# Performance work log

Measured on AMD Instinct MI355X. Metric: run time of the kernel, lower is better.

The kernel has to match this reference:

```python
import jax, jax.numpy as jnp
import numpy as np

# BERT-base dims; 768 and max_sent_num=64 come from the module/config.
N, S, V, D, L, H, F = 8, 512, 30522, 768, 12, 12, 3072
DH = D // H
MAX_SENT = 64
LN_EPS = 1e-12
SCALE = float(np.sqrt(DH))


def _ln(x, g, b):
    m = jnp.mean(x, axis=-1, keepdims=True)
    v = jnp.mean(jnp.square(x - m), axis=-1, keepdims=True)
    return (x - m) * jax.lax.rsqrt(v + LN_EPS) * g + b


def setup_inputs() -> dict:
    key = jax.random.key(0)
    ks = jax.random.split(key, 10)
    # random token ids in a range avoiding the special ids 102/103
    ids = jax.random.randint(ks[0], (N, S), 999, 30000, dtype=jnp.int32)
    # variable per-doc sentence region -> ragged number of [MASK](103) separators (8..64)
    cutoff = jax.random.randint(ks[1], (N, 1), 64, S + 1)
    pos = jnp.arange(S)[None, :]
    sent_pos = ((pos % 8) == 7) & (pos < cutoff)
    ids = jnp.where(sent_pos, 103, ids)
    ids = ids.at[:, 0].set(102)  # exactly one [SEP]=102 per doc (required by the slice-assign)
    amask = jnp.ones((N, S), dtype=jnp.int32)
    g = lambda k, shape: 0.02 * jax.random.normal(k, shape, dtype=jnp.float32)
    inp = dict(input_ids_bert=ids, attention_mask_bert=amask)
    inp["tok_emb"] = g(ks[2], (V, D))
    inp["pos_emb"] = g(ks[3], (S, D))
    inp["emb_ln_g"] = jnp.ones((D,), jnp.float32)
    inp["emb_ln_b"] = jnp.zeros((D,), jnp.float32)
    inp["Wqkv"] = g(ks[4], (L, D, 3 * D))
    inp["bqkv"] = jnp.zeros((L, 3 * D), jnp.float32)
    inp["Wo"] = g(ks[5], (L, D, D))
    inp["bo"] = jnp.zeros((L, D), jnp.float32)
    inp["ln1_g"] = jnp.ones((L, D), jnp.float32)
    inp["ln1_b"] = jnp.zeros((L, D), jnp.float32)
    inp["W1"] = g(ks[6], (L, D, F))
    inp["b1"] = jnp.zeros((L, F), jnp.float32)
    inp["W2"] = g(ks[7], (L, F, D))
    inp["b2"] = jnp.zeros((L, D), jnp.float32)
    inp["ln2_g"] = jnp.ones((L, D), jnp.float32)
    inp["ln2_b"] = jnp.zeros((L, D), jnp.float32)
    return inp


def _bert(ids, amask, tok_emb, pos_emb, emb_ln_g, emb_ln_b,
          Wqkv, bqkv, Wo, bo, ln1_g, ln1_b, W1, b1, W2, b2, ln2_g, ln2_b):
    x = tok_emb[ids] + pos_emb[None, :, :]            # [N,S,D]
    x = _ln(x, emb_ln_g, emb_ln_b)
    bias = (1.0 - amask[:, None, None, :].astype(x.dtype)) * -1e9  # [N,1,1,S]

    def layer(x, p):
        wqkv, bq, wo, bo_, g1, b1n, w1, b1f, w2, b2f, g2, b2n = p
        qkv = x @ wqkv + bq
        q, k, v = jnp.split(qkv, 3, axis=-1)
        q = q.reshape(N, S, H, DH)
        k = k.reshape(N, S, H, DH)
        v = v.reshape(N, S, H, DH)
        att = jnp.einsum('bqhd,bkhd->bhqk', q, k) / SCALE + bias
        att = jax.nn.softmax(att, axis=-1)
        o = jnp.einsum('bhqk,bkhd->bqhd', att, v).reshape(N, S, D)
        x2 = _ln(x + o @ wo + bo_, g1, b1n)
        h = jax.nn.gelu(x2 @ w1 + b1f, approximate=False)
        return _ln(x2 + h @ w2 + b2f, g2, b2n), None

    x, _ = jax.lax.scan(layer, x, (Wqkv, bqkv, Wo, bo, ln1_g, ln1_b, W1, b1, W2, b2, ln2_g, ln2_b))
    return x


def _gather_scatter(ids, h):
    # Vectorized form of the per-doc python loop:
    #   out[doc, :n_sent] = concat([cls_emb(102), sent_embs(103)])[:-1]
    mask_sent = ids == 103
    mask_cls = ids == 102
    n_cls = mask_cls.sum(axis=1, keepdims=True)              # == 1 per doc
    total_sent = mask_sent.sum(axis=1, keepdims=True)        # ragged count
    rank_sent = jnp.cumsum(mask_sent, axis=1) - 1
    rank_cls = jnp.cumsum(mask_cls, axis=1) - 1
    dest = jnp.where(mask_cls, rank_cls,
                     jnp.where(mask_sent, n_cls + rank_sent, MAX_SENT))
    valid = (mask_cls | mask_sent) & (dest < total_sent) & (dest < MAX_SENT)
    dest_safe = jnp.where(valid, dest, MAX_SENT)             # dump invalid into scratch row
    vals = jnp.where(valid[..., None], h, 0.0)
    out = jnp.zeros((ids.shape[0], MAX_SENT + 1, D), dtype=h.dtype)
    out = out.at[jnp.arange(ids.shape[0])[:, None], dest_safe].set(vals)
    return out[:, :MAX_SENT]


def reference(input_ids_bert, attention_mask_bert, tok_emb, pos_emb, emb_ln_g, emb_ln_b,
              Wqkv, bqkv, Wo, bo, ln1_g, ln1_b, W1, b1, W2, b2, ln2_g, ln2_b):
    h = _bert(input_ids_bert, attention_mask_bert, tok_emb, pos_emb, emb_ln_g, emb_ln_b,
              Wqkv, bqkv, Wo, bo, ln1_g, ln1_b, W1, b1, W2, b2, ln2_g, ln2_b)
    return _gather_scatter(input_ids_bert, h)
```

## Files before the change

### kernel.cpp

```cpp
#include <hip/hip_runtime.h>
#include <hip/hip_bf16.h>

#define DEV static __device__ __forceinline__

using short8 = __attribute__((ext_vector_type(8))) short;
using f32x4 = __attribute__((ext_vector_type(4))) float;

DEV short f2bf(float f) {
  union { float f; unsigned u; } x; x.f = f;
  unsigned r = x.u + 0x7fffu + ((x.u >> 16) & 1u);
  return (short)(r >> 16);
}

DEV float bf2f(short s) {
  union { unsigned u; float f; } x; x.u = ((unsigned)(unsigned short)s) << 16;
  return x.f;
}

DEV void gload16(const void* g, void* lds) {
  __builtin_amdgcn_global_load_lds(
      (const __attribute__((address_space(1))) void*)g,
      (__attribute__((address_space(3))) void*)lds, 16, 0, 0);
}

__global__ __launch_bounds__(256) void transpose_all_k(
    const float* __restrict__ Wqkv, const float* __restrict__ Wo,
    const float* __restrict__ W1, const float* __restrict__ W2,
    short* __restrict__ wqkvT, short* __restrict__ woT,
    short* __restrict__ w1T, short* __restrict__ w2T)
{
  __shared__ short t[64][72];
  const int b = blockIdx.x, tid = threadIdx.x;
  const float* in; short* out; int K, N, tt, nt;
  if (b < 432)       { in = Wqkv; out = wqkvT; K = 768;  N = 2304; tt = b;        nt = 36; }
  else if (b < 576)  { in = Wo;   out = woT;   K = 768;  N = 768;  tt = b - 432;  nt = 12; }
  else if (b < 1152) { in = W1;   out = w1T;   K = 768;  N = 3072; tt = b - 576;  nt = 48; }
  else               { in = W2;   out = w2T;   K = 3072; N = 768;  tt = b - 1152; nt = 12; }
  const int n0 = (tt % nt) * 64, k0 = (tt / nt) * 64;
  #pragma unroll
  for (int p = 0; p < 4; ++p) {
    int r = p * 16 + (tid >> 4), c4 = tid & 15;
    float4 v = *reinterpret_cast<const float4*>(in + (size_t)(k0 + r) * N + n0 + c4 * 4);
    t[r][c4 * 4 + 0] = f2bf(v.x);
    t[r][c4 * 4 + 1] = f2bf(v.y);
    t[r][c4 * 4 + 2] = f2bf(v.z);
    t[r][c4 * 4 + 3] = f2bf(v.w);
  }
  __syncthreads();
  #pragma unroll
  for (int q = 0; q < 2; ++q) {
    int n = tid >> 2, kc = (tid & 3) + q * 4;
    short8 o;
    #pragma unroll
    for (int j = 0; j < 8; ++j) o[j] = t[kc * 8 + j][n];
    *reinterpret_cast<short8*>(out + (size_t)(n0 + n) * K + k0 + kc * 8) = o;
  }
}

template <int BM, int EPI>
__global__ __launch_bounds__(256) void gemm_bt(
    const short* __restrict__ A, const short* __restrict__ Bt,
    const float* __restrict__ bias, const float* __restrict__ resid,
    void* __restrict__ Cout, int M, int Nn, int K)
{
  constexpr int AW = BM / 64;
  constexpr int MI = BM / 32;
  __shared__ short As[2 * BM * 32];
  __shared__ short Bs[2 * 128 * 32];
  const int tid = threadIdx.x, lane = tid & 63, w = tid >> 6;
  const int wr = w >> 1, wc = w & 1;
  const int l15 = lane & 15, l4 = lane >> 4;
  const int m0 = blockIdx.y * BM, n0 = blockIdx.x * 128;
  const int crow = lane >> 2, ccol = (lane & 3) * 8;

  f32x4 acc[MI][4] = {};

  for (int k0 = 0; k0 < K; k0 += 64) {
    #pragma unroll
    for (int ks = 0; ks < 2; ++ks) {
      #pragma unroll
      for (int s = 0; s < AW; ++s) {
        int c = w * AW + s;
        gload16(A + (size_t)(m0 + c * 16 + crow) * K + k0 + ks * 32 + ccol,
                &As[ks * BM * 32 + c * 512]);
      }
      #pragma unroll
      for (int s = 0; s < 2; ++s) {
        int c = w * 2 + s;
        gload16(Bt + (size_t)(n0 + c * 16 + crow) * K + k0 + ks * 32 + ccol,
                &Bs[ks * 128 * 32 + c * 512]);
      }
    }
    __syncthreads();

    #pragma unroll
    for (int ks = 0; ks < 2; ++ks) {
      short8 af[MI], bfr[4];
      #pragma unroll
      for (int i = 0; i < MI; ++i)
        af[i] = *reinterpret_cast<const short8*>(
            &As[ks * BM * 32 + (wr * (BM / 2) + i * 16 + l15) * 32 + l4 * 8]);
      #pragma unroll
      for (int j = 0; j < 4; ++j)
        bfr[j] = *reinterpret_cast<const short8*>(
            &Bs[ks * 128 * 32 + (wc * 64 + j * 16 + l15) * 32 + l4 * 8]);
      #pragma unroll
      for (int i = 0; i < MI; ++i)
        #pragma unroll
        for (int j = 0; j < 4; ++j)
          acc[i][j] = __builtin_amdgcn_mfma_f32_16x16x32_bf16(af[i], bfr[j], acc[i][j], 0, 0, 0);
    }
    __syncthreads();
  }

  #pragma unroll
  for (int i = 0; i < MI; ++i) {
    #pragma unroll
    for (int j = 0; j < 4; ++j) {
      #pragma unroll
      for (int r = 0; r < 4; ++r) {
        int row = m0 + wr * (BM / 2) + i * 16 + l4 * 4 + r;
        int col = n0 + wc * 64 + j * 16 + l15;
        float v = acc[i][j][r] + bias[col];
        if constexpr (EPI == 1) v = 0.5f * v * (1.0f + erff(v * 0.70710678118654752f));
        ((short*)Cout)[(size_t)row * Nn + col] = f2bf(v);
      }
    }
  }
}

__global__ __launch_bounds__(256) void gemm_sk(
    const short* __restrict__ A, const short* __restrict__ Bt,
    short* __restrict__ p0, short* __restrict__ p1,
    short* __restrict__ p2, short* __restrict__ p3,
    int M, int Nn, int Kstride, int Klen)
{
  __shared__ short As[2 * 128 * 32];
  __shared__ short Bs[2 * 128 * 32];
  const int tid = threadIdx.x, lane = tid & 63, w = tid >> 6;
  const int wr = w >> 1, wc = w & 1;
  const int l15 = lane & 15, l4 = lane >> 4;
  const int m0 = blockIdx.y * 128, n0 = blockIdx.x * 128;
  const int koff = blockIdx.z * Klen;
  const int crow = lane >> 2, ccol = (lane & 3) * 8;

  f32x4 acc[4][4] = {};

  for (int k0 = 0; k0 < Klen; k0 += 64) {
    #pragma unroll
    for (int ks = 0; ks < 2; ++ks) {
      #pragma unroll
      for (int s = 0; s < 2; ++s) {
        int c = w * 2 + s;
        gload16(A + (size_t)(m0 + c * 16 + crow) * Kstride + koff + k0 + ks * 32 + ccol,
                &As[ks * 4096 + c * 512]);
      }
      #pragma unroll
      for (int s = 0; s < 2; ++s) {
        int c = w * 2 + s;
        gload16(Bt + (size_t)(n0 + c * 16 + crow) * Kstride + koff + k0 + ks * 32 + ccol,
                &Bs[ks * 4096 + c * 512]);
      }
    }
    __syncthreads();

    #pragma unroll
    for (int ks = 0; ks < 2; ++ks) {
      short8 af[4], bfr[4];
      #pragma unroll
      for (int i = 0; i < 4; ++i)
        af[i] = *reinterpret_cast<const short8*>(
            &As[ks * 4096 + (wr * 64 + i * 16 + l15) * 32 + l4 * 8]);
      #pragma unroll
      for (int j = 0; j < 4; ++j)
        bfr[j] = *reinterpret_cast<const short8*>(
            &Bs[ks * 4096 + (wc * 64 + j * 16 + l15) * 32 + l4 * 8]);
      #pragma unroll
      for (int i = 0; i < 4; ++i)
        #pragma unroll
        for (int j = 0; j < 4; ++j)
          acc[i][j] = __builtin_amdgcn_mfma_f32_16x16x32_bf16(af[i], bfr[j], acc[i][j], 0, 0, 0);
    }
    __syncthreads();
  }

  short* P = (blockIdx.z == 0) ? p0 : (blockIdx.z == 1) ? p1 : (blockIdx.z == 2) ? p2 : p3;
  #pragma unroll
  for (int i = 0; i < 4; ++i)
    #pragma unroll
    for (int j = 0; j < 4; ++j)
      #pragma unroll
      for (int r = 0; r < 4; ++r) {
        int row = m0 + wr * 64 + i * 16 + l4 * 4 + r;
        int col = n0 + wc * 64 + j * 16 + l15;
        P[(size_t)row * Nn + col] = f2bf(acc[i][j][r]);
      }
}

__global__ __launch_bounds__(256) void attn_k(
    const short* __restrict__ qkv, const int* __restrict__ amask,
    short* __restrict__ out)
{
  __shared__ short Kl[64][72];
  __shared__ short Vt[64][68];
  __shared__ short Pl[4][16][72];
  const int b = blockIdx.z, h = blockIdx.y, qt = blockIdx.x;
  const int tid = threadIdx.x, lane = tid & 63, w = tid >> 6;
  const int l15 = lane & 15, l4 = lane >> 4;
  const int tok0 = b * 512;
  const int q0 = qt * 64 + w * 16;

  short8 qf[2];
  #pragma unroll
  for (int kk = 0; kk < 2; ++kk)
    qf[kk] = *reinterpret_cast<const short8*>(
        qkv + (size_t)(tok0 + q0 + l15) * 2304 + h * 64 + kk * 32 + l4 * 8);

  f32x4 oacc[4] = {};
  float mrow[4], lrow[4];
  #pragma unroll
  for (int r = 0; r < 4; ++r) { mrow[r] = -1e30f; lrow[r] = 0.f; }

  for (int kt0 = 0; kt0 < 512; kt0 += 64) {
    #pragma unroll
    for (int i = 0; i < 2; ++i) {
      int c = tid + i * 256;
      int r = c >> 3, dc = c & 7;
      short8 v = *reinterpret_cast<const short8*>(
          qkv + (size_t)(tok0 + kt0 + r) * 2304 + 768 + h * 64 + dc * 8);
      *reinterpret_cast<short8*>(&Kl[r][dc * 8]) = v;
    }
    #pragma unroll
    for (int i = 0; i < 2; ++i) {
      int c = tid + i * 256;
      int r = c >> 3, dc = c & 7;
      short8 v = *reinterpret_cast<const short8*>(
          qkv + (size_t)(tok0 + kt0 + r) * 2304 + 1536 + h * 64 + dc * 8);
      #pragma unroll
      for (int j = 0; j < 8; ++j) Vt[dc * 8 + j][r] = v[j];
    }
    __syncthreads();

    f32x4 sacc[4] = {};
    #pragma unroll
    for (int t = 0; t < 4; ++t) {
      #pragma unroll
      for (int kk = 0; kk < 2; ++kk) {
        short8 kf = *reinterpret_cast<const short8*>(&Kl[t * 16 + l15][kk * 32 + l4 * 8]);
        sacc[t] = __builtin_amdgcn_mfma_f32_16x16x32_bf16(qf[kk], kf, sacc[t], 0, 0, 0);
      }
    }
    float p[4][4];
    #pragma unroll
    for (int t = 0; t < 4; ++t) {
      int ktok = kt0 + t * 16 + l15;
      float biasv = amask[b * 512 + ktok] ? 0.f : -1e9f;
      #pragma unroll
      for (int r = 0; r < 4; ++r) p[t][r] = sacc[t][r] * 0.125f + biasv;
    }
    #pragma unroll
    for (int r = 0; r < 4; ++r) {
      float mx = fmaxf(fmaxf(p[0][r], p[1][r]), fmaxf(p[2][r], p[3][r]));
      #pragma unroll
      for (int s = 1; s <= 8; s <<= 1) mx = fmaxf(mx, __shfl_xor(mx, s, 64));
      float mnew = fmaxf(mrow[r], mx);
      float alpha = __expf(mrow[r] - mnew);
      mrow[r] = mnew;
      float sum = 0.f;
      #pragma unroll
      for (int t = 0; t < 4; ++t) { p[t][r] = __expf(p[t][r] - mnew); sum += p[t][r]; }
      #pragma unroll
      for (int s = 1; s <= 8; s <<= 1) sum += __shfl_xor(sum, s, 64);
      lrow[r] = lrow[r] * alpha + sum;
      #pragma unroll
      for (int t = 0; t < 4; ++t) oacc[t][r] *= alpha;
    }
    #pragma unroll
    for (int t = 0; t < 4; ++t)
      #pragma unroll
      for (int r = 0; r < 4; ++r)
        Pl[w][l4 * 4 + r][t * 16 + l15] = f2bf(p[t][r]);
    #pragma unroll
    for (int kk = 0; kk < 2; ++kk) {
      short8 pf = *reinterpret_cast<const short8*>(&Pl[w][l15][kk * 32 + l4 * 8]);
      #pragma unroll
      for (int t = 0; t < 4; ++t) {
        const unsigned* vp = reinterpret_cast<const unsigned*>(&Vt[t * 16 + l15][0]);
        union { short8 s; unsigned u[4]; } vu;
        #pragma unroll
        for (int w2 = 0; w2 < 4; ++w2) vu.u[w2] = vp[kk * 16 + l4 * 4 + w2];
        oacc[t] = __builtin_amdgcn_mfma_f32_16x16x32_bf16(pf, vu.s, oacc[t], 0, 0, 0);
      }
    }
    __syncthreads();
  }

  #pragma unroll
  for (int t = 0; t < 4; ++t)
    #pragma unroll
    for (int r = 0; r < 4; ++r) {
      int tok = tok0 + q0 + l4 * 4 + r;
      int dh = t * 16 + l15;
      out[(size_t)tok * 768 + h * 64 + dh] = f2bf(oacc[t][r] / lrow[r]);
    }
}

__global__ __launch_bounds__(256) void ln2_k(
    const short* __restrict__ p0, const short* __restrict__ p1,
    const short* __restrict__ p2, const short* __restrict__ p3,
    const float* __restrict__ bias, const float* __restrict__ resid,
    const float* __restrict__ g, const float* __restrict__ be,
    float* __restrict__ xf, short* __restrict__ xb)
{
  const int t = blockIdx.x, tid = threadIdx.x;
  const size_t base = (size_t)t * 768;
  float v[3], s = 0.f, ss = 0.f;
  #pragma unroll
  for (int i = 0; i < 3; ++i) {
    int c = tid + i * 256;
    v[i] = (bf2f(p0[base + c]) + bf2f(p1[base + c]))
         + (bf2f(p2[base + c]) + bf2f(p3[base + c]))
         + bias[c] + resid[base + c];
    s += v[i]; ss += v[i] * v[i];
  }
  __shared__ float red[4][2];
  #pragma unroll
  for (int m = 1; m <= 32; m <<= 1) { s += __shfl_xor(s, m, 64); ss += __shfl_xor(ss, m, 64); }
  int w = tid >> 6;
  if ((tid & 63) == 0) { red[w][0] = s; red[w][1] = ss; }
  __syncthreads();
  s = red[0][0] + red[1][0] + red[2][0] + red[3][0];
  ss = red[0][1] + red[1][1] + red[2][1] + red[3][1];
  float mean = s * (1.f / 768.f);
  float var = ss * (1.f / 768.f) - mean * mean;
  float rs = rsqrtf(var + 1e-12f);
  #pragma unroll
  for (int i = 0; i < 3; ++i) {
    int c = tid + i * 256;
    float o = (v[i] - mean) * rs * g[c] + be[c];
    xf[base + c] = o;
    xb[base + c] = f2bf(o);
  }
}

__global__ __launch_bounds__(256) void embed_ln_k(
    const int* __restrict__ ids, const float* __restrict__ tok_emb,
    const float* __restrict__ pos_emb, const float* __restrict__ g,
    const float* __restrict__ be, float* __restrict__ xf, short* __restrict__ xb)
{
  const int t = blockIdx.x, tid = threadIdx.x;
  const int id = ids[t], sp = t & 511;
  float v[3], s = 0.f, ss = 0.f;
  #pragma unroll
  for (int i = 0; i < 3; ++i) {
    int c = tid + i * 256;
    v[i] = tok_emb[(size_t)id * 768 + c] + pos_emb[(size_t)sp * 768 + c];
    s += v[i]; ss += v[i] * v[i];
  }
  __shared__ float red[4][2];
  #pragma unroll
  for (int m = 1; m <= 32; m <<= 1) { s += __shfl_xor(s, m, 64); ss += __shfl_xor(ss, m, 64); }
  int w = tid >> 6;
  if ((tid & 63) == 0) { red[w][0] = s; red[w][1] = ss; }
  __syncthreads();
  s = red[0][0] + red[1][0] + red[2][0] + red[3][0];
  ss = red[0][1] + red[1][1] + red[2][1] + red[3][1];
  float mean = s * (1.f / 768.f);
  float var = ss * (1.f / 768.f) - mean * mean;
  float rs = rsqrtf(var + 1e-12f);
  #pragma unroll
  for (int i = 0; i < 3; ++i) {
    int c = tid + i * 256;
    float o = (v[i] - mean) * rs * g[c] + be[c];
    xf[(size_t)t * 768 + c] = o;
    xb[(size_t)t * 768 + c] = f2bf(o);
  }
}

__global__ __launch_bounds__(512) void gather_k(
    const int* __restrict__ ids, const float* __restrict__ x, float* __restrict__ out)
{
  const int doc = blockIdx.x, tid = threadIdx.x;
  const int lane = tid & 63, w = tid >> 6;
  __shared__ int src[64];
  __shared__ int wave_sent[8];
  __shared__ int cls_pos;
  if (tid < 64) src[tid] = -1;
  if (tid == 0) cls_pos = 0x7fffffff;
  __syncthreads();

  const int id = ids[doc * 512 + tid];
  const bool is_sent = (id == 103);
  const unsigned long long m = __ballot(is_sent);
  if (lane == 0) wave_sent[w] = __popcll(m);
  if (id == 102) atomicMin(&cls_pos, tid);
  __syncthreads();

  int total = 0, prefix = 0;
  #pragma unroll
  for (int i = 0; i < 8; ++i) {
    int c = wave_sent[i];
    if (i < w) prefix += c;
    total += c;
  }
  if (is_sent) {
    unsigned long long lt = lane ? (~0ULL >> (64 - lane)) : 0ULL;
    int d = 1 + prefix + __popcll(m & lt);
    if (d < total && d < 64) src[d] = tid;
  }
  if (tid == 0 && total > 0 && cls_pos != 0x7fffffff) src[0] = cls_pos;
  __syncthreads();

  for (int i = tid; i < 64 * 192; i += 512) {
    int row = i / 192, c4 = i - row * 192;
    int sp = src[row];
    float4 v = make_float4(0.f, 0.f, 0.f, 0.f);
    if (sp >= 0)
      v = reinterpret_cast<const float4*>(x + (size_t)(doc * 512 + sp) * 768)[c4];
    reinterpret_cast<float4*>(out + (size_t)doc * 64 * 768)[i] = v;
  }
}

extern "C" void kernel_launch(void* const* d_in, const int* in_sizes, int n_in,
                              void* d_out, int out_size, void* d_ws, size_t ws_size,
                              hipStream_t stream)
{
  const int* ids = (const int*)d_in[0];
  const int* am = (const int*)d_in[1];
  const float* tok_emb = (const float*)d_in[2];
  const float* pos_emb = (const float*)d_in[3];
  const float* eg = (const float*)d_in[4];
  const float* eb = (const float*)d_in[5];
  const float* Wqkv = (const float*)d_in[6];
  const float* bqkv = (const float*)d_in[7];
  const float* Wo = (const float*)d_in[8];
  const float* bo = (const float*)d_in[9];
  const float* g1 = (const float*)d_in[10];
  const float* b1n = (const float*)d_in[11];
  const float* W1 = (const float*)d_in[12];
  const float* b1f = (const float*)d_in[13];
  const float* W2 = (const float*)d_in[14];
  const float* b2f = (const float*)d_in[15];
  const float* g2 = (const float*)d_in[16];
  const float* b2n = (const float*)d_in[17];

  char* ws = (char*)d_ws;
  float* x_f   = (float*)(ws);
  short* x_b   = (short*)(ws + 12582912);
  float* x2_f  = (float*)(ws + 18874368);
  short* x2_b  = (short*)(ws + 31457280);
  short* pp0   = (short*)(ws + 37748736);
  short* pp1   = (short*)(ws + 37748736 + 6291456);
  short* qkv   = (short*)(ws + 50331648);
  short* pp2   = (short*)(ws + 50331648);
  short* pp3   = (short*)(ws + 50331648 + 6291456);
  short* attn  = (short*)(ws + 69206016);
  short* hb    = (short*)(ws + 75497472);
  short* wqkvT = (short*)(ws + 100663296);
  short* woT   = (short*)(ws + 104202240);
  short* w1T   = (short*)(ws + 105381888);
  short* w2T   = (short*)(ws + 110100480);

  embed_ln_k<<<4096, 256, 0, stream>>>(ids, tok_emb, pos_emb, eg, eb, x_f, x_b);

  for (int l = 0; l < 12; ++l) {
    transpose_all_k<<<1728, 256, 0, stream>>>(
        Wqkv + (size_t)l * 768 * 2304, Wo + (size_t)l * 768 * 768,
        W1 + (size_t)l * 768 * 3072, W2 + (size_t)l * 3072 * 768,
        wqkvT, woT, w1T, w2T);

    gemm_bt<128, 0><<<dim3(18, 32), 256, 0, stream>>>(
        x_b, wqkvT, bqkv + (size_t)l * 2304, nullptr, qkv, 4096, 2304, 768);
    attn_k<<<dim3(8, 12, 8), 256, 0, stream>>>(qkv, am, attn);

    gemm_sk<<<dim3(6, 32, 4), 256, 0, stream>>>(
        attn, woT, pp0, pp1, pp2, pp3, 4096, 768, 768, 192);
    ln2_k<<<4096, 256, 0, stream>>>(
        pp0, pp1, pp2, pp3, bo + (size_t)l * 768, x_f,
        g1 + (size_t)l * 768, b1n + (size_t)l * 768, x2_f, x2_b);

    gemm_bt<128, 1><<<dim3(24, 32), 256, 0, stream>>>(
        x2_b, w1T, b1f + (size_t)l * 3072, nullptr, hb, 4096, 3072, 768);

    gemm_sk<<<dim3(6, 32, 4), 256, 0, stream>>>(
        hb, w2T, pp0, pp1, pp2, pp3, 4096, 768, 3072, 768);
    ln2_k<<<4096, 256, 0, stream>>>(
        pp0, pp1, pp2, pp3, b2f + (size_t)l * 768, x2_f,
        g2 + (size_t)l * 768, b2n + (size_t)l * 768, x_f, x_b);
  }

  gather_k<<<8, 512, 0, stream>>>(ids, x_f, (float*)d_out);
}
```

Measured before the change: 2.208 ms.

## Batch weight transposes, swizzle workgroups across XCDs, use fast erf in GELU

When the workspace is large enough, all 12 layers' weights are transposed to bf16 in one launch up front, replacing a transpose launch per layer. GEMM and attention kernels remap their block indices with an XCD-aware swizzle so that neighbouring tiles land on the same chiplet and share L2. The GELU epilogue swaps erff for an Abramowitz-Stegun polynomial using a fast exp. The costs are a large extra workspace, a small loss of erf accuracy, and a swizzle that assumes the block count divides evenly by 8.

```diff
diff --git a/kernel.cpp b/kernel.cpp
--- a/kernel.cpp
+++ b/kernel.cpp
@@ -21,6 +21,50 @@
   __builtin_amdgcn_global_load_lds(
       (const __attribute__((address_space(1))) void*)g,
       (__attribute__((address_space(3))) void*)lds, 16, 0, 0);
+}
+
+DEV float erf_fast(float x) {
+  float ax = fabsf(x);
+  float t = __fdividef(1.f, 1.f + 0.3275911f * ax);
+  float y = t * (0.254829592f + t * (-0.284496736f +
+            t * (1.421413741f + t * (-1.453152027f + t * 1.061405429f))));
+  float r = 1.f - y * __expf(-ax * ax);
+  return copysignf(r, x);
+}
+
+DEV void swz_grid(int& bx, int& by, int& bz) {
+  const int nx = gridDim.x, ny = gridDim.y;
+  const int nwg = nx * ny * (int)gridDim.z;
+  const int lin = (int)blockIdx.x + nx * ((int)blockIdx.y + ny * (int)blockIdx.z);
+  const int cpx = nwg >> 3;
+  const int s = (lin & 7) * cpx + (lin >> 3);
+  bx = s % nx;
+  const int t = s / nx;
+  by = t % ny;
+  bz = t / ny;
+}
+
+DEV void transpose_tile(const float* in, short* out, int K, int N, int tt, int nt,
+                        int tid, short (*t)[72]) {
+  const int n0 = (tt % nt) * 64, k0 = (tt / nt) * 64;
+  #pragma unroll
+  for (int p = 0; p < 4; ++p) {
+    int r = p * 16 + (tid >> 4), c4 = tid & 15;
+    float4 v = *reinterpret_cast<const float4*>(in + (size_t)(k0 + r) * N + n0 + c4 * 4);
+    t[r][c4 * 4 + 0] = f2bf(v.x);
+    t[r][c4 * 4 + 1] = f2bf(v.y);
+    t[r][c4 * 4 + 2] = f2bf(v.z);
+    t[r][c4 * 4 + 3] = f2bf(v.w);
+  }
+  __syncthreads();
+  #pragma unroll
+  for (int q = 0; q < 2; ++q) {
+    int n = tid >> 2, kc = (tid & 3) + q * 4;
+    short8 o;
+    #pragma unroll
+    for (int j = 0; j < 8; ++j) o[j] = t[kc * 8 + j][n];
+    *reinterpret_cast<short8*>(out + (size_t)(n0 + n) * K + k0 + kc * 8) = o;
+  }
 }
 
 __global__ __launch_bounds__(256) void transpose_all_k(
@@ -36,25 +80,23 @@
   else if (b < 576)  { in = Wo;   out = woT;   K = 768;  N = 768;  tt = b - 432;  nt = 12; }
   else if (b < 1152) { in = W1;   out = w1T;   K = 768;  N = 3072; tt = b - 576;  nt = 48; }
   else               { in = W2;   out = w2T;   K = 3072; N = 768;  tt = b - 1152; nt = 12; }
-  const int n0 = (tt % nt) * 64, k0 = (tt / nt) * 64;
-  #pragma unroll
-  for (int p = 0; p < 4; ++p) {
-    int r = p * 16 + (tid >> 4), c4 = tid & 15;
-    float4 v = *reinterpret_cast<const float4*>(in + (size_t)(k0 + r) * N + n0 + c4 * 4);
-    t[r][c4 * 4 + 0] = f2bf(v.x);
-    t[r][c4 * 4 + 1] = f2bf(v.y);
-    t[r][c4 * 4 + 2] = f2bf(v.z);
-    t[r][c4 * 4 + 3] = f2bf(v.w);
-  }
-  __syncthreads();
-  #pragma unroll
-  for (int q = 0; q < 2; ++q) {
-    int n = tid >> 2, kc = (tid & 3) + q * 4;
-    short8 o;
-    #pragma unroll
-    for (int j = 0; j < 8; ++j) o[j] = t[kc * 8 + j][n];
-    *reinterpret_cast<short8*>(out + (size_t)(n0 + n) * K + k0 + kc * 8) = o;
-  }
+  transpose_tile(in, out, K, N, tt, nt, tid, t);
+}
+
+__global__ __launch_bounds__(256) void transpose12_k(
+    const float* __restrict__ Wqkv, const float* __restrict__ Wo,
+    const float* __restrict__ W1, const float* __restrict__ W2,
+    short* __restrict__ wqkvT, short* __restrict__ woT,
+    short* __restrict__ w1T, short* __restrict__ w2T)
+{
+  __shared__ short t[64][72];
+  const int b = blockIdx.x, l = blockIdx.z, tid = threadIdx.x;
+  const float* in; short* out; int K, N, tt, nt;
+  if (b < 432)       { in = Wqkv + (size_t)l * 768 * 2304; out = wqkvT + (size_t)l * 2304 * 768; K = 768;  N = 2304; tt = b;        nt = 36; }
+  else if (b < 576)  { in = Wo   + (size_t)l * 768 * 768;  out = woT   + (size_t)l * 768 * 768;  K = 768;  N = 768;  tt = b - 432;  nt = 12; }
+  else if (b < 1152) { in = W1   + (size_t)l * 768 * 3072; out = w1T   + (size_t)l * 3072 * 768; K = 768;  N = 3072; tt = b - 576;  nt = 48; }
+  else               { in = W2   + (size_t)l * 3072 * 768; out = w2T   + (size_t)l * 768 * 3072; K = 3072; N = 768;  tt = b - 1152; nt = 12; }
+  transpose_tile(in, out, K, N, tt, nt, tid, t);
 }
 
 template <int BM, int EPI>
@@ -67,10 +109,12 @@
   constexpr int MI = BM / 32;
   __shared__ short As[2 * BM * 32];
   __shared__ short Bs[2 * 128 * 32];
+  int bx, by, bz;
+  swz_grid(bx, by, bz);
   const int tid = threadIdx.x, lane = tid & 63, w = tid >> 6;
   const int wr = w >> 1, wc = w & 1;
   const int l15 = lane & 15, l4 = lane >> 4;
-  const int m0 = blockIdx.y * BM, n0 = blockIdx.x * 128;
+  const int m0 = by * BM, n0 = bx * 128;
   const int crow = lane >> 2, ccol = (lane & 3) * 8;
 
   f32x4 acc[MI][4] = {};
@@ -122,7 +166,7 @@
         int row = m0 + wr * (BM / 2) + i * 16 + l4 * 4 + r;
         int col = n0 + wc * 64 + j * 16 + l15;
         float v = acc[i][j][r] + bias[col];
-        if constexpr (EPI == 1) v = 0.5f * v * (1.0f + erff(v * 0.70710678118654752f));
+        if constexpr (EPI == 1) v = 0.5f * v * (1.0f + erf_fast(v * 0.70710678118654752f));
         ((short*)Cout)[(size_t)row * Nn + col] = f2bf(v);
       }
     }
@@ -137,11 +181,13 @@
 {
   __shared__ short As[2 * 128 * 32];
   __shared__ short Bs[2 * 128 * 32];
+  int bx, by, bz;
+  swz_grid(bx, by, bz);
   const int tid = threadIdx.x, lane = tid & 63, w = tid >> 6;
   const int wr = w >> 1, wc = w & 1;
   const int l15 = lane & 15, l4 = lane >> 4;
-  const int m0 = blockIdx.y * 128, n0 = blockIdx.x * 128;
-  const int koff = blockIdx.z * Klen;
+  const int m0 = by * 128, n0 = bx * 128;
+  const int koff = bz * Klen;
   const int crow = lane >> 2, ccol = (lane & 3) * 8;
 
   f32x4 acc[4][4] = {};
@@ -184,7 +230,7 @@
     __syncthreads();
   }
 
-  short* P = (blockIdx.z == 0) ? p0 : (blockIdx.z == 1) ? p1 : (blockIdx.z == 2) ? p2 : p3;
+  short* P = (bz == 0) ? p0 : (bz == 1) ? p1 : (bz == 2) ? p2 : p3;
   #pragma unroll
   for (int i = 0; i < 4; ++i)
     #pragma unroll
@@ -204,7 +250,9 @@
   __shared__ short Kl[64][72];
   __shared__ short Vt[64][68];
   __shared__ short Pl[4][16][72];
-  const int b = blockIdx.z, h = blockIdx.y, qt = blockIdx.x;
+  int bx, by, bz;
+  swz_grid(bx, by, bz);
+  const int b = bz, h = by, qt = bx;
   const int tid = threadIdx.x, lane = tid & 63, w = tid >> 6;
   const int l15 = lane & 15, l4 = lane >> 4;
   const int tok0 = b * 512;
@@ -456,34 +504,55 @@
   short* pp3   = (short*)(ws + 50331648 + 6291456);
   short* attn  = (short*)(ws + 69206016);
   short* hb    = (short*)(ws + 75497472);
+  const size_t WQ = 2304ull * 768, WO = 768ull * 768, W1S = 3072ull * 768, W2S = 768ull * 3072;
+  const size_t NEED_ALL = 100663296ull + 12ull * (WQ + WO + W1S + W2S) * 2ull;
+  const bool big = ws_size >= NEED_ALL;
+
   short* wqkvT = (short*)(ws + 100663296);
-  short* woT   = (short*)(ws + 104202240);
-  short* w1T   = (short*)(ws + 105381888);
-  short* w2T   = (short*)(ws + 110100480);
+  short* woT, *w1T, *w2T;
+  if (big) {
+    woT = wqkvT + 12 * WQ;
+    w1T = woT + 12 * WO;
+    w2T = w1T + 12 * W1S;
+  } else {
+    woT = (short*)(ws + 104202240);
+    w1T = (short*)(ws + 105381888);
+    w2T = (short*)(ws + 110100480);
+  }
 
   embed_ln_k<<<4096, 256, 0, stream>>>(ids, tok_emb, pos_emb, eg, eb, x_f, x_b);
 
+  if (big)
+    transpose12_k<<<dim3(1728, 1, 12), 256, 0, stream>>>(
+        Wqkv, Wo, W1, W2, wqkvT, woT, w1T, w2T);
+
   for (int l = 0; l < 12; ++l) {
-    transpose_all_k<<<1728, 256, 0, stream>>>(
-        Wqkv + (size_t)l * 768 * 2304, Wo + (size_t)l * 768 * 768,
-        W1 + (size_t)l * 768 * 3072, W2 + (size_t)l * 3072 * 768,
-        wqkvT, woT, w1T, w2T);
+    short *wq, *wo, *w1, *w2;
+    if (big) {
+      wq = wqkvT + l * WQ; wo = woT + l * WO; w1 = w1T + l * W1S; w2 = w2T + l * W2S;
+    } else {
+      transpose_all_k<<<1728, 256, 0, stream>>>(
+          Wqkv + (size_t)l * 768 * 2304, Wo + (size_t)l * 768 * 768,
+          W1 + (size_t)l * 768 * 3072, W2 + (size_t)l * 3072 * 768,
+          wqkvT, woT, w1T, w2T);
+      wq = wqkvT; wo = woT; w1 = w1T; w2 = w2T;
+    }
 
     gemm_bt<128, 0><<<dim3(18, 32), 256, 0, stream>>>(
-        x_b, wqkvT, bqkv + (size_t)l * 2304, nullptr, qkv, 4096, 2304, 768);
+        x_b, wq, bqkv + (size_t)l * 2304, nullptr, qkv, 4096, 2304, 768);
     attn_k<<<dim3(8, 12, 8), 256, 0, stream>>>(qkv, am, attn);
 
     gemm_sk<<<dim3(6, 32, 4), 256, 0, stream>>>(
-        attn, woT, pp0, pp1, pp2, pp3, 4096, 768, 768, 192);
+        attn, wo, pp0, pp1, pp2, pp3, 4096, 768, 768, 192);
     ln2_k<<<4096, 256, 0, stream>>>(
         pp0, pp1, pp2, pp3, bo + (size_t)l * 768, x_f,
         g1 + (size_t)l * 768, b1n + (size_t)l * 768, x2_f, x2_b);
 
     gemm_bt<128, 1><<<dim3(24, 32), 256, 0, stream>>>(
-        x2_b, w1T, b1f + (size_t)l * 3072, nullptr, hb, 4096, 3072, 768);
+        x2_b, w1, b1f + (size_t)l * 3072, nullptr, hb, 4096, 3072, 768);
 
     gemm_sk<<<dim3(6, 32, 4), 256, 0, stream>>>(
-        hb, w2T, pp0, pp1, pp2, pp3, 4096, 768, 3072, 768);
+        hb, w2, pp0, pp1, pp2, pp3, 4096, 768, 3072, 768);
     ln2_k<<<4096, 256, 0, stream>>>(
         pp0, pp1, pp2, pp3, b2f + (size_t)l * 768, x2_f,
         g2 + (size_t)l * 768, b2n + (size_t)l * 768, x_f, x_b);
```

After: 2.240 ms. Within noise of the previous version (+1.4%).
